# Kernel tuning notes

Measured on AMD Instinct MI355X. Metric: run time of the kernel, lower is better.

## Reference

```python
import jax, jax.numpy as jnp
import numpy as np

B, C, H, NP, M = 32, 768, 12, 196, 64
D = C // H
GRID = 14  # sqrt(196)
NG = 1 + NP  # cls + patches = 197
EPS = 1e-5


def _ln(x, w, b):
    mu = x.mean(-1, keepdims=True)
    var = ((x - mu) ** 2).mean(-1, keepdims=True)
    return (x - mu) * jax.lax.rsqrt(var + EPS) * w + b


def setup_inputs() -> dict:
    key = jax.random.key(0)
    ks = jax.random.split(key, 14)
    std = 0.02
    return {
        "x": jax.random.normal(ks[0], (B, NG + M, C), dtype=jnp.float32),
        "ps": jax.random.uniform(ks[1], (B, M, 2), dtype=jnp.float32) * 224.0,
        "ns": jax.random.randint(ks[2], (B,), 1, M + 1, dtype=jnp.int32),
        "norm1_w": jnp.ones((C,), jnp.float32),
        "norm1_b": jnp.zeros((C,), jnp.float32),
        "qkv_w": jax.random.normal(ks[3], (3 * C, C), jnp.float32) * std,
        "proj_w": jax.random.normal(ks[4], (C, C), jnp.float32) * std,
        "proj_b": jnp.zeros((C,), jnp.float32),
        "norm2_w": jnp.ones((C,), jnp.float32),
        "norm2_b": jnp.zeros((C,), jnp.float32),
        "fc1_w": jax.random.normal(ks[5], (4 * C, C), jnp.float32) * std,
        "fc1_b": jnp.zeros((4 * C,), jnp.float32),
        "fc2_w": jax.random.normal(ks[6], (C, 4 * C), jnp.float32) * std,
        "fc2_b": jnp.zeros((C,), jnp.float32),
    }


def reference(x, ps, ns, norm1_w, norm1_b, qkv_w, proj_w, proj_b,
              norm2_w, norm2_b, fc1_w, fc1_b, fc2_w, fc2_b):
    Bn, Nt, Cd = x.shape  # Nt = 1 + 196 + M
    scale = D ** -0.5

    h = _ln(x, norm1_w, norm1_b)
    qkv = (h @ qkv_w.T).reshape(Bn, Nt, 3, H, D).transpose(2, 0, 3, 1, 4)  # [3,B,H,Nt,D]
    q, k, v = qkv[0], qkv[1], qkv[2]

    # ---- global attention over cls + patch tokens (first 197) ----
    attn = jnp.einsum('bhnd,bhmd->bhnm', q[:, :, :NG], k[:, :, :NG]) * scale
    attn = jax.nn.softmax(attn, axis=-1)
    xg = jnp.einsum('bhnm,bhmd->bhnd', attn, v[:, :, :NG])
    xg = xg.transpose(0, 2, 1, 3).reshape(Bn, NG, Cd)  # [B,197,C]

    # ---- keypoint bilinear-gather attention (get_single_filter_matrix) ----
    pos = ps / 16.0  # [B,M,2]; pos[...,1] -> row (dim 4), pos[...,0] -> col (dim 5)
    c0 = jnp.clip(jnp.floor(pos[..., 0]), 0, GRID - 1).astype(jnp.int32)
    c1 = jnp.clip(jnp.ceil(pos[..., 0]), 0, GRID - 1).astype(jnp.int32)
    r0 = jnp.clip(jnp.floor(pos[..., 1]), 0, GRID - 1).astype(jnp.int32)
    r1 = jnp.clip(jnp.ceil(pos[..., 1]), 0, GRID - 1).astype(jnp.int32)
    # neighbor order: top_left, top_right, bottom_left, bottom_right
    rows = jnp.stack([r0, r1, r0, r1], axis=-1)  # [B,M,4]
    cols = jnp.stack([c0, c0, c1, c1], axis=-1)
    flat = rows * GRID + cols  # [B,M,4] flat index into 196 patch tokens

    kp = k[:, :, 1:NG]  # [B,H,196,D]
    vp = v[:, :, 1:NG]
    idx = jnp.broadcast_to(flat.reshape(Bn, 1, M * 4, 1), (Bn, H, M * 4, D))
    knb = jnp.take_along_axis(kp, idx, axis=2).reshape(Bn, H, M, 4, D)
    vnb = jnp.take_along_axis(vp, idx, axis=2).reshape(Bn, H, M, 4, D)

    qk = q[:, :, NG:]  # keypoint queries [B,H,M,D]
    a = jnp.einsum('bhmd,bhmjd->bhmj', qk, knb)  # no scale, per original
    a = jax.nn.softmax(a, axis=-1)
    kout = jnp.einsum('bhmj,bhmjd->bhmd', a, vnb)
    kout = kout.transpose(0, 2, 1, 3).reshape(Bn, M, Cd)

    y = jnp.concatenate([xg, kout], axis=1) @ proj_w.T + proj_b
    x = x + y

    h2 = _ln(x, norm2_w, norm2_b)
    h2 = jax.nn.gelu(h2 @ fc1_w.T + fc1_b, approximate=False)
    x = x + (h2 @ fc2_w.T + fc2_b)
    return x
```

## Files before the change

kernel.cpp:

```cpp
#include <hip/hip_runtime.h>

typedef unsigned short u16;
typedef unsigned int u32;
typedef u16 u16x8 __attribute__((ext_vector_type(8)));
typedef u16 u16x4 __attribute__((ext_vector_type(4)));
typedef float f32x4 __attribute__((ext_vector_type(4)));
typedef __bf16 bf16x8 __attribute__((ext_vector_type(8)));

#define NHEAD 12
#define NT 261
#define NGL 197
#define CDIM 768
#define KT 14
#define PS_STRIDE 232
#define VT_STRIDE 232

__device__ __forceinline__ float bf2f(u16 u) {
    u32 x = ((u32)u) << 16;
    float f;
    __builtin_memcpy(&f, &x, 4);
    return f;
}
__device__ __forceinline__ u16 f2bf(float f) {
    u32 x;
    __builtin_memcpy(&x, &f, 4);
    x = (x + 0x7fffu + ((x >> 16) & 1u)) >> 16;
    return (u16)x;
}

#define GLD_LDS16(g, l) \
    __builtin_amdgcn_global_load_lds((const __attribute__((address_space(1))) void*)(g), \
                                     (__attribute__((address_space(3))) void*)(l), 16, 0, 0)
#define WAITV(n) asm volatile("s_waitcnt vmcnt(" #n ")" ::: "memory")
#define BARM() asm volatile("s_barrier" ::: "memory")

struct CvArgs {
    const float* in[4];
    u16* out[4];
    int n4[4];
};

__device__ __forceinline__ void ln_row(const float* __restrict__ in, const float* __restrict__ w,
                                       const float* __restrict__ bia, u16* __restrict__ out,
                                       int row, int lane) {
    const float4* r = (const float4*)(in + (size_t)row * CDIM);
    float4 a = r[lane], b4 = r[lane + 64], c4 = r[lane + 128];
    float s  = a.x + a.y + a.z + a.w + b4.x + b4.y + b4.z + b4.w + c4.x + c4.y + c4.z + c4.w;
    float ss = a.x*a.x + a.y*a.y + a.z*a.z + a.w*a.w
             + b4.x*b4.x + b4.y*b4.y + b4.z*b4.z + b4.w*b4.w
             + c4.x*c4.x + c4.y*c4.y + c4.z*c4.z + c4.w*c4.w;
#pragma unroll
    for (int off = 32; off; off >>= 1) {
        s  += __shfl_xor(s, off);
        ss += __shfl_xor(ss, off);
    }
    float mu = s * (1.f / 768.f);
    float var = ss * (1.f / 768.f) - mu * mu;
    float inv = rsqrtf(var + 1e-5f);
    const float4* wp = (const float4*)w;
    const float4* bp = (const float4*)bia;
    u16* o = out + (size_t)row * CDIM;
#pragma unroll
    for (int t = 0; t < 3; ++t) {
        float4 v = (t == 0) ? a : (t == 1) ? b4 : c4;
        float4 ww = wp[lane + t * 64], bb = bp[lane + t * 64];
        u16x4 ov;
        ov[0] = f2bf((v.x - mu) * inv * ww.x + bb.x);
        ov[1] = f2bf((v.y - mu) * inv * ww.y + bb.y);
        ov[2] = f2bf((v.z - mu) * inv * ww.z + bb.z);
        ov[3] = f2bf((v.w - mu) * inv * ww.w + bb.w);
        *(u16x4*)(o + t * 256 + lane * 4) = ov;
    }
}

__global__ __launch_bounds__(256) void pre_k(const float* __restrict__ x, const float* __restrict__ w,
                                             const float* __restrict__ bia, u16* __restrict__ out,
                                             int nrows, CvArgs cv) {
    if (blockIdx.y == 0) {
        int i = blockIdx.x * 256 + threadIdx.x;
        int s0 = cv.n4[0], s1 = s0 + cv.n4[1], s2 = s1 + cv.n4[2], s3 = s2 + cv.n4[3];
        const float* in;
        u16* o;
        int base;
        if (i < s0)      { in = cv.in[0]; o = cv.out[0]; base = 0; }
        else if (i < s1) { in = cv.in[1]; o = cv.out[1]; base = s0; }
        else if (i < s2) { in = cv.in[2]; o = cv.out[2]; base = s1; }
        else if (i < s3) { in = cv.in[3]; o = cv.out[3]; base = s2; }
        else return;
        int j = i - base;
        float4 v = ((const float4*)in)[j];
        u16x4 ov;
        ov[0] = f2bf(v.x); ov[1] = f2bf(v.y); ov[2] = f2bf(v.z); ov[3] = f2bf(v.w);
        ((u16x4*)o)[j] = ov;
    } else {
        int lane = threadIdx.x & 63, wv = threadIdx.x >> 6;
        int row = blockIdx.x * 4 + wv;
        if (row < nrows) ln_row(x, w, bia, out, row, lane);
    }
}

__global__ __launch_bounds__(256) void ln_w(const float* __restrict__ in, const float* __restrict__ w,
                                            const float* __restrict__ bia, u16* __restrict__ out, int nrows) {
    int lane = threadIdx.x & 63, wv = threadIdx.x >> 6;
    int row = blockIdx.x * 4 + wv;
    if (row < nrows) ln_row(in, w, bia, out, row, lane);
}

template <int EPI>
__global__ __launch_bounds__(256, 4) void gemm11(const u16* __restrict__ A, const u16* __restrict__ Bw,
                                                 int M, int N, int K, int nbn,
                                                 const float* __restrict__ bias,
                                                 const float* __restrict__ resid, void* __restrict__ outp) {
    __shared__ __align__(16) u16 sm[2][8192];
    const int tid = threadIdx.x;
    const int nwg = gridDim.x;
    const int q = nwg >> 3, r = nwg & 7;
    const int xcd = blockIdx.x & 7, within = blockIdx.x >> 3;
    const int id2 = (xcd < r ? xcd * (q + 1) : r * (q + 1) + (xcd - r) * q) + within;
    const int bm = id2 / nbn, bn = id2 % nbn;
    const int lane = tid & 63, wv = tid >> 6;
    const int wr = wv >> 1, wc = wv & 1;
    const int l15 = lane & 15, lg = lane >> 4;
    const int arow0 = bm * 128, brow0 = bn * 128;
    const int nt = K >> 5;

    const int srow = tid >> 2;
    const int sslot = tid & 3;
    const int sk = (sslot ^ ((srow >> 1) & 3)) * 8;
    const u16* gA[2];
    const u16* gB[2];
#pragma unroll
    for (int i = 0; i < 2; ++i) {
        int ar = arow0 + i * 64 + srow;
        if (ar >= M) ar = M - 1;
        gA[i] = A + (size_t)ar * K + sk;
        gB[i] = Bw + (size_t)(brow0 + i * 64 + srow) * K + sk;
    }

    auto STAGE = [&](int tt) {
        u16* sb = sm[tt & 1];
        const size_t ko = (size_t)tt * 32;
#pragma unroll
        for (int i = 0; i < 2; ++i) GLD_LDS16(gA[i] + ko, sb + i * 2048 + tid * 8);
#pragma unroll
        for (int i = 0; i < 2; ++i) GLD_LDS16(gB[i] + ko, sb + 4096 + i * 2048 + tid * 8);
    };

    f32x4 acc[4][4] = {};
    const int xb = (l15 >> 1) & 3;

    STAGE(0);
    for (int t = 0; t < nt; ++t) {
        if (t + 1 < nt) {
            STAGE(t + 1);
            WAITV(4);
        } else {
            WAITV(0);
        }
        BARM();
        const u16* sb = sm[t & 1];
        bf16x8 af[4], bq[4];
#pragma unroll
        for (int mi = 0; mi < 4; ++mi)
            af[mi] = *(const bf16x8*)(sb + (wr * 64 + mi * 16 + l15) * 32 + ((lg ^ xb) * 8));
#pragma unroll
        for (int ni = 0; ni < 4; ++ni)
            bq[ni] = *(const bf16x8*)(sb + 4096 + (wc * 64 + ni * 16 + l15) * 32 + ((lg ^ xb) * 8));
#pragma unroll
        for (int mi = 0; mi < 4; ++mi)
#pragma unroll
            for (int ni = 0; ni < 4; ++ni)
                acc[mi][ni] = __builtin_amdgcn_mfma_f32_16x16x32_bf16(af[mi], bq[ni], acc[mi][ni], 0, 0, 0);
        if (t + 2 < nt) BARM();
    }

#pragma unroll
    for (int mi = 0; mi < 4; ++mi) {
        int row0 = arow0 + wr * 64 + mi * 16 + lg * 4;
#pragma unroll
        for (int ni = 0; ni < 4; ++ni) {
            int col = brow0 + wc * 64 + ni * 16 + l15;
            float bb = (EPI == 0) ? 0.f : bias[col];
#pragma unroll
            for (int rr = 0; rr < 4; ++rr) {
                int row = row0 + rr;
                if (row < M) {
                    float v = acc[mi][ni][rr] + bb;
                    if (EPI == 2) {
                        float z = v + 0.044715f * v * v * v;
                        v = v / (1.f + __expf(-1.5957691216f * z));
                    }
                    ((u16*)outp)[(size_t)row * N + col] = f2bf(v);
                }
            }
        }
    }
}

__global__ __launch_bounds__(256, 4) void gemm12(const u16* __restrict__ A, const u16* __restrict__ Bw,
                                                 int M, int N, int K, int nbn,
                                                 const float* __restrict__ bias,
                                                 const float* __restrict__ resid, void* __restrict__ outp) {
    __shared__ __align__(16) u16 sm[2][6144];
    const int tid = threadIdx.x;
    const int nwg = gridDim.x;
    const int q = nwg >> 3, r = nwg & 7;
    const int xcd = blockIdx.x & 7, within = blockIdx.x >> 3;
    const int id2 = (xcd < r ? xcd * (q + 1) : r * (q + 1) + (xcd - r) * q) + within;
    const int bm = id2 / nbn, bn = id2 % nbn;
    const int lane = tid & 63, wv = tid >> 6;
    const int wr = wv >> 1, wc = wv & 1;
    const int l15 = lane & 15, lg = lane >> 4;
    const int arow0 = bm * 64, brow0 = bn * 128;
    const int nt = K >> 5;

    const int srow = tid >> 2;
    const int sslot = tid & 3;
    const int sk = (sslot ^ ((srow >> 1) & 3)) * 8;
    int ar0 = arow0 + srow; if (ar0 >= M) ar0 = M - 1;
    const u16* gA0 = A + (size_t)ar0 * K + sk;
    const u16* gB[2];
#pragma unroll
    for (int i = 0; i < 2; ++i)
        gB[i] = Bw + (size_t)(brow0 + i * 64 + srow) * K + sk;

    auto STAGE = [&](int tt) {
        u16* sb = sm[tt & 1];
        const size_t ko = (size_t)tt * 32;
        GLD_LDS16(gA0 + ko, sb + tid * 8);
#pragma unroll
        for (int i = 0; i < 2; ++i) GLD_LDS16(gB[i] + ko, sb + 2048 + i * 2048 + tid * 8);
    };

    f32x4 acc[2][4] = {};
    const int xb = (l15 >> 1) & 3;

    STAGE(0);
    for (int t = 0; t < nt; ++t) {
        if (t + 1 < nt) {
            STAGE(t + 1);
            WAITV(3);
        } else {
            WAITV(0);
        }
        BARM();
        const u16* sb = sm[t & 1];
        bf16x8 af[2], bq[4];
#pragma unroll
        for (int mi = 0; mi < 2; ++mi)
            af[mi] = *(const bf16x8*)(sb + (wr * 32 + mi * 16 + l15) * 32 + ((lg ^ xb) * 8));
#pragma unroll
        for (int ni = 0; ni < 4; ++ni)
            bq[ni] = *(const bf16x8*)(sb + 2048 + (wc * 64 + ni * 16 + l15) * 32 + ((lg ^ xb) * 8));
#pragma unroll
        for (int mi = 0; mi < 2; ++mi)
#pragma unroll
            for (int ni = 0; ni < 4; ++ni)
                acc[mi][ni] = __builtin_amdgcn_mfma_f32_16x16x32_bf16(af[mi], bq[ni], acc[mi][ni], 0, 0, 0);
        if (t + 2 < nt) BARM();
    }

#pragma unroll
    for (int mi = 0; mi < 2; ++mi) {
        int row0 = arow0 + wr * 32 + mi * 16 + lg * 4;
#pragma unroll
        for (int ni = 0; ni < 4; ++ni) {
            int col = brow0 + wc * 64 + ni * 16 + l15;
            float bb = bias[col];
#pragma unroll
            for (int rr = 0; rr < 4; ++rr) {
                int row = row0 + rr;
                if (row < M) {
                    float v = acc[mi][ni][rr] + bb + resid[(size_t)row * N + col];
                    ((float*)outp)[(size_t)row * N + col] = v;
                }
            }
        }
    }
}

__global__ __launch_bounds__(256) void attn_fused(const u16* __restrict__ qkv, const float* __restrict__ ps,
                                                  u16* __restrict__ Z) {
    __shared__ __align__(16) u16 lds0[4 * 16 * PS_STRIDE];
    __shared__ __align__(16) u16 Vt[64 * VT_STRIDE];
    const int tid = threadIdx.x;
    const int lane = tid & 63, wv = tid >> 6;

    if (blockIdx.x >= 1536) {
        int idx = blockIdx.x - 1536;
        int b = idx >> 4;
        int m = (idx & 15) * 4 + wv;
        float px = ps[((size_t)b * 64 + m) * 2 + 0] * (1.f / 16.f);
        float py = ps[((size_t)b * 64 + m) * 2 + 1] * (1.f / 16.f);
        int c0 = min(max((int)floorf(px), 0), 13);
        int c1 = min(max((int)ceilf(px), 0), 13);
        int r0 = min(max((int)floorf(py), 0), 13);
        int r1 = min(max((int)ceilf(py), 0), 13);
        int tok[4];
        tok[0] = 1 + r0 * 14 + c0;
        tok[1] = 1 + r1 * 14 + c0;
        tok[2] = 1 + r0 * 14 + c1;
        tok[3] = 1 + r1 * 14 + c1;
        const size_t rowq = ((size_t)b * NT + NGL + m) * 2304;
#pragma unroll 1
        for (int h = 0; h < NHEAD; ++h) {
            float qv = bf2f(qkv[rowq + h * 64 + lane]);
            float a[4];
#pragma unroll
            for (int j = 0; j < 4; ++j) {
                float p = qv * bf2f(qkv[((size_t)b * NT + tok[j]) * 2304 + 768 + h * 64 + lane]);
#pragma unroll
                for (int off = 32; off; off >>= 1) p += __shfl_xor(p, off);
                a[j] = p;
            }
            float mx = fmaxf(fmaxf(a[0], a[1]), fmaxf(a[2], a[3]));
            float e0 = expf(a[0] - mx), e1 = expf(a[1] - mx), e2 = expf(a[2] - mx), e3 = expf(a[3] - mx);
            float inv = 1.f / (e0 + e1 + e2 + e3);
            float v0 = bf2f(qkv[((size_t)b * NT + tok[0]) * 2304 + 1536 + h * 64 + lane]);
            float v1 = bf2f(qkv[((size_t)b * NT + tok[1]) * 2304 + 1536 + h * 64 + lane]);
            float v2 = bf2f(qkv[((size_t)b * NT + tok[2]) * 2304 + 1536 + h * 64 + lane]);
            float v3 = bf2f(qkv[((size_t)b * NT + tok[3]) * 2304 + 1536 + h * 64 + lane]);
            float o = (e0 * v0 + e1 * v1 + e2 * v2 + e3 * v3) * inv;
            Z[((size_t)b * NT + NGL + m) * CDIM + h * 64 + lane] = f2bf(o);
        }
        return;
    }

    const int blk = blockIdx.x;
    const int qt = blk & 3;
    const int bh = blk >> 2;
    const int h = bh % NHEAD, b = bh / NHEAD;
    const int l15 = lane & 15, lg = lane >> 4;
    const u16* base = qkv + (size_t)b * NT * 2304;

    for (int c = tid; c < 224 * 8; c += 256) {
        int row = c >> 3, ch = c & 7;
        u16x8 v = {};
        if (row < NGL) v = *(const u16x8*)(base + (size_t)row * 2304 + 768 + h * 64 + ch * 8);
        int byte = row * 128 + ((ch * 16) ^ ((row & 7) << 4));
        *(u16x8*)((char*)lds0 + byte) = v;
    }
    for (int c = tid; c < 112 * 8; c += 256) {
        int mp = c >> 3, dch = c & 7;
        int m0 = mp * 2;
        u16x8 a0 = {}, a1 = {};
        if (m0 < NGL)     a0 = *(const u16x8*)(base + (size_t)m0 * 2304 + 1536 + h * 64 + dch * 8);
        if (m0 + 1 < NGL) a1 = *(const u16x8*)(base + (size_t)(m0 + 1) * 2304 + 1536 + h * 64 + dch * 8);
#pragma unroll
        for (int j = 0; j < 8; ++j) {
            u32 pk = (u32)a0[j] | ((u32)a1[j] << 16);
            *(u32*)((char*)Vt + (size_t)(dch * 8 + j) * (VT_STRIDE * 2) + m0 * 2) = pk;
        }
    }
    const int q0 = qt * 64 + wv * 16;
    int qrow = q0 + l15; if (qrow > NGL - 1) qrow = NGL - 1;
    bf16x8 aq0 = *(const bf16x8*)(base + (size_t)qrow * 2304 + h * 64 + lg * 8);
    bf16x8 aq1 = *(const bf16x8*)(base + (size_t)qrow * 2304 + h * 64 + 32 + lg * 8);
    __syncthreads();

    f32x4 s[KT];
    const int sw = (l15 & 7) << 4;
#pragma unroll
    for (int t = 0; t < KT; ++t) {
        const char* krow = (const char*)lds0 + (t * 16 + l15) * 128;
        bf16x8 bk0 = *(const bf16x8*)(krow + ((lg * 16) ^ sw));
        bf16x8 bk1 = *(const bf16x8*)(krow + ((64 + lg * 16) ^ sw));
        f32x4 acc = {};
        acc = __builtin_amdgcn_mfma_f32_16x16x32_bf16(aq0, bk0, acc, 0, 0, 0);
        acc = __builtin_amdgcn_mfma_f32_16x16x32_bf16(aq1, bk1, acc, 0, 0, 0);
        s[t] = acc * 0.125f;
    }
    float mx[4] = {-1e30f, -1e30f, -1e30f, -1e30f};
#pragma unroll
    for (int t = 0; t < KT; ++t)
#pragma unroll
        for (int r = 0; r < 4; ++r) mx[r] = fmaxf(mx[r], s[t][r]);
#pragma unroll
    for (int off = 1; off < 16; off <<= 1)
#pragma unroll
        for (int r = 0; r < 4; ++r) mx[r] = fmaxf(mx[r], __shfl_xor(mx[r], off));
    float sum[4] = {};
#pragma unroll
    for (int t = 0; t < KT; ++t) {
        bool valid = (t * 16 + l15) < NGL;
#pragma unroll
        for (int r = 0; r < 4; ++r) {
            float e = valid ? __expf(s[t][r] - mx[r]) : 0.f;
            s[t][r] = e;
            sum[r] += e;
        }
    }
#pragma unroll
    for (int off = 1; off < 16; off <<= 1)
#pragma unroll
        for (int r = 0; r < 4; ++r) sum[r] += __shfl_xor(sum[r], off);
    float inv[4];
#pragma unroll
    for (int r = 0; r < 4; ++r) inv[r] = 1.f / sum[r];

    __syncthreads();
    u16* Pw = lds0 + wv * 16 * PS_STRIDE;
#pragma unroll
    for (int t = 0; t < KT; ++t)
#pragma unroll
        for (int r = 0; r < 4; ++r)
            Pw[(4 * lg + r) * PS_STRIDE + t * 16 + l15] = f2bf(s[t][r] * inv[r]);

    f32x4 o[4] = {};
#pragma unroll
    for (int ks = 0; ks < 7; ++ks) {
        bf16x8 pa = *(const bf16x8*)(Pw + l15 * PS_STRIDE + ks * 32 + lg * 8);
#pragma unroll
        for (int dt = 0; dt < 4; ++dt) {
            bf16x8 bv = *(const bf16x8*)((const char*)Vt + (size_t)(dt * 16 + l15) * (VT_STRIDE * 2) + ks * 64 + lg * 16);
            o[dt] = __builtin_amdgcn_mfma_f32_16x16x32_bf16(pa, bv, o[dt], 0, 0, 0);
        }
    }
#pragma unroll
    for (int dt = 0; dt < 4; ++dt)
#pragma unroll
        for (int r = 0; r < 4; ++r) {
            int q = q0 + 4 * lg + r;
            if (q < NGL) Z[((size_t)b * NT + q) * CDIM + h * 64 + dt * 16 + l15] = f2bf(o[dt][r]);
        }
}

extern "C" void kernel_launch(void* const* d_in, const int* in_sizes, int n_in,
                              void* d_out, int out_size, void* d_ws, size_t ws_size,
                              hipStream_t stream) {
    const float* x      = (const float*)d_in[0];
    const float* ps     = (const float*)d_in[1];
    const float* n1w    = (const float*)d_in[3];
    const float* n1b    = (const float*)d_in[4];
    const float* qkv_w  = (const float*)d_in[5];
    const float* proj_w = (const float*)d_in[6];
    const float* proj_b = (const float*)d_in[7];
    const float* n2w    = (const float*)d_in[8];
    const float* n2b    = (const float*)d_in[9];
    const float* fc1_w  = (const float*)d_in[10];
    const float* fc1_b  = (const float*)d_in[11];
    const float* fc2_w  = (const float*)d_in[12];
    const float* fc2_b  = (const float*)d_in[13];

    char* ws = (char*)d_ws;
    const int M = 32 * NT;
    u16* hbuf  = (u16*)ws;
    u16* qkvb  = (u16*)(ws + 12828672);
    u16* Zb    = (u16*)(ws + 12828672 + 38486016);
    u16* Gb    = (u16*)(ws + 12828672);
    float* x1  = (float*)(ws + 64143360);
    u16* wq    = (u16*)(ws + 89800704);
    u16* wp    = wq + 2304 * 768;
    u16* w1    = wp + 768 * 768;
    u16* w2    = w1 + 3072 * 768;

    CvArgs cv;
    cv.in[0] = qkv_w;  cv.out[0] = wq; cv.n4[0] = 2304 * 768 / 4;
    cv.in[1] = proj_w; cv.out[1] = wp; cv.n4[1] = 768 * 768 / 4;
    cv.in[2] = fc1_w;  cv.out[2] = w1; cv.n4[2] = 3072 * 768 / 4;
    cv.in[3] = fc2_w;  cv.out[3] = w2; cv.n4[3] = 768 * 3072 / 4;

    pre_k<<<dim3(6912, 2), 256, 0, stream>>>(x, n1w, n1b, hbuf, M, cv);
    gemm11<0><<<66 * 18, 256, 0, stream>>>(hbuf, wq, M, 2304, 768, 18, nullptr, nullptr, qkvb);
    attn_fused<<<2048, 256, 0, stream>>>(qkvb, ps, Zb);
    gemm12<<<131 * 6, 256, 0, stream>>>(Zb, wp, M, 768, 768, 6, proj_b, x, x1);
    ln_w<<<2088, 256, 0, stream>>>(x1, n2w, n2b, hbuf, M);
    gemm11<2><<<66 * 24, 256, 0, stream>>>(hbuf, w1, M, 3072, 768, 24, fc1_b, nullptr, Gb);
    gemm12<<<131 * 6, 256, 0, stream>>>(Gb, w2, M, 768, 3072, 6, fc2_b, x1, (float*)d_out);
}
```

Before: 304.2 us.

## Skip unused K/V rows in QKV GEMM, store residual x1 as bf16

The QKV projection becomes a dedicated kernel. Q is computed for all 261 tokens, but K and V only for the 197 global tokens, using a row remap (row/197*261 + row%197), because keypoint tokens never serve as keys or values. The proj and fc2 GEMMs move from 64-row tiles to the 128-row gemm11 tiles, and the intermediate residual x1 is stored in bf16 rather than fp32, with a bf16-input LayerNorm to match. This cuts MMA work and memory traffic, but rounding the residual stream to bf16 costs precision, and the larger tiles give fewer blocks for the N=768 GEMMs.

```diff
diff --git a/kernel.cpp b/kernel.cpp
--- a/kernel.cpp
+++ b/kernel.cpp
@@ -69,6 +69,43 @@
         ov[1] = f2bf((v.y - mu) * inv * ww.y + bb.y);
         ov[2] = f2bf((v.z - mu) * inv * ww.z + bb.z);
         ov[3] = f2bf((v.w - mu) * inv * ww.w + bb.w);
+        *(u16x4*)(o + t * 256 + lane * 4) = ov;
+    }
+}
+
+__device__ __forceinline__ void ln_row_bf(const u16* __restrict__ in, const float* __restrict__ w,
+                                          const float* __restrict__ bia, u16* __restrict__ out,
+                                          int row, int lane) {
+    const u16* r = in + (size_t)row * CDIM;
+    float v[12];
+#pragma unroll
+    for (int t = 0; t < 3; ++t) {
+        u16x4 u = *(const u16x4*)(r + t * 256 + lane * 4);
+#pragma unroll
+        for (int j = 0; j < 4; ++j) v[t * 4 + j] = bf2f(u[j]);
+    }
+    float s = 0.f, ss = 0.f;
+#pragma unroll
+    for (int j = 0; j < 12; ++j) { s += v[j]; ss += v[j] * v[j]; }
+#pragma unroll
+    for (int off = 32; off; off >>= 1) {
+        s  += __shfl_xor(s, off);
+        ss += __shfl_xor(ss, off);
+    }
+    float mu = s * (1.f / 768.f);
+    float var = ss * (1.f / 768.f) - mu * mu;
+    float inv = rsqrtf(var + 1e-5f);
+    const float4* wp = (const float4*)w;
+    const float4* bp = (const float4*)bia;
+    u16* o = out + (size_t)row * CDIM;
+#pragma unroll
+    for (int t = 0; t < 3; ++t) {
+        float4 ww = wp[lane + t * 64], bb = bp[lane + t * 64];
+        u16x4 ov;
+        ov[0] = f2bf((v[t * 4 + 0] - mu) * inv * ww.x + bb.x);
+        ov[1] = f2bf((v[t * 4 + 1] - mu) * inv * ww.y + bb.y);
+        ov[2] = f2bf((v[t * 4 + 2] - mu) * inv * ww.z + bb.z);
+        ov[3] = f2bf((v[t * 4 + 3] - mu) * inv * ww.w + bb.w);
         *(u16x4*)(o + t * 256 + lane * 4) = ov;
     }
 }
@@ -99,18 +136,18 @@
     }
 }
 
-__global__ __launch_bounds__(256) void ln_w(const float* __restrict__ in, const float* __restrict__ w,
-                                            const float* __restrict__ bia, u16* __restrict__ out, int nrows) {
+__global__ __launch_bounds__(256) void ln_wbf(const u16* __restrict__ in, const float* __restrict__ w,
+                                              const float* __restrict__ bia, u16* __restrict__ out, int nrows) {
     int lane = threadIdx.x & 63, wv = threadIdx.x >> 6;
     int row = blockIdx.x * 4 + wv;
-    if (row < nrows) ln_row(in, w, bia, out, row, lane);
+    if (row < nrows) ln_row_bf(in, w, bia, out, row, lane);
 }
 
 template <int EPI>
 __global__ __launch_bounds__(256, 4) void gemm11(const u16* __restrict__ A, const u16* __restrict__ Bw,
                                                  int M, int N, int K, int nbn,
                                                  const float* __restrict__ bias,
-                                                 const float* __restrict__ resid, void* __restrict__ outp) {
+                                                 const void* __restrict__ resid, void* __restrict__ outp) {
     __shared__ __align__(16) u16 sm[2][8192];
     const int tid = threadIdx.x;
     const int nwg = gridDim.x;
@@ -180,80 +217,95 @@
 #pragma unroll
         for (int ni = 0; ni < 4; ++ni) {
             int col = brow0 + wc * 64 + ni * 16 + l15;
-            float bb = (EPI == 0) ? 0.f : bias[col];
+            float bb = bias[col];
 #pragma unroll
             for (int rr = 0; rr < 4; ++rr) {
                 int row = row0 + rr;
                 if (row < M) {
                     float v = acc[mi][ni][rr] + bb;
-                    if (EPI == 2) {
+                    if (EPI == 1) {
+                        v += ((const float*)resid)[(size_t)row * N + col];
+                        ((u16*)outp)[(size_t)row * N + col] = f2bf(v);
+                    } else if (EPI == 2) {
                         float z = v + 0.044715f * v * v * v;
                         v = v / (1.f + __expf(-1.5957691216f * z));
+                        ((u16*)outp)[(size_t)row * N + col] = f2bf(v);
+                    } else {
+                        v += bf2f(((const u16*)resid)[(size_t)row * N + col]);
+                        ((float*)outp)[(size_t)row * N + col] = v;
                     }
-                    ((u16*)outp)[(size_t)row * N + col] = f2bf(v);
                 }
             }
         }
     }
 }
 
-__global__ __launch_bounds__(256, 4) void gemm12(const u16* __restrict__ A, const u16* __restrict__ Bw,
-                                                 int M, int N, int K, int nbn,
-                                                 const float* __restrict__ bias,
-                                                 const float* __restrict__ resid, void* __restrict__ outp) {
-    __shared__ __align__(16) u16 sm[2][6144];
+__global__ __launch_bounds__(256, 4) void gemm_qkv(const u16* __restrict__ A, const u16* __restrict__ Bw,
+                                                   u16* __restrict__ outp) {
+    __shared__ __align__(16) u16 sm[2][8192];
     const int tid = threadIdx.x;
     const int nwg = gridDim.x;
     const int q = nwg >> 3, r = nwg & 7;
     const int xcd = blockIdx.x & 7, within = blockIdx.x >> 3;
     const int id2 = (xcd < r ? xcd * (q + 1) : r * (q + 1) + (xcd - r) * q) + within;
-    const int bm = id2 / nbn, bn = id2 % nbn;
+    const bool kvz = (id2 >= 396);
+    const int idz = kvz ? id2 - 396 : id2;
+    const int bm = kvz ? idz / 12 : idz / 6;
+    const int bn = kvz ? idz % 12 : idz % 6;
+    const int Mz = kvz ? 6304 : 8352;
+    const int colbase = kvz ? 768 + bn * 128 : bn * 128;
     const int lane = tid & 63, wv = tid >> 6;
     const int wr = wv >> 1, wc = wv & 1;
     const int l15 = lane & 15, lg = lane >> 4;
-    const int arow0 = bm * 64, brow0 = bn * 128;
-    const int nt = K >> 5;
+    const int arow0 = bm * 128;
+    const int K = 768;
+    const int nt = 24;
 
     const int srow = tid >> 2;
     const int sslot = tid & 3;
     const int sk = (sslot ^ ((srow >> 1) & 3)) * 8;
-    int ar0 = arow0 + srow; if (ar0 >= M) ar0 = M - 1;
-    const u16* gA0 = A + (size_t)ar0 * K + sk;
+    const u16* gA[2];
     const u16* gB[2];
 #pragma unroll
-    for (int i = 0; i < 2; ++i)
-        gB[i] = Bw + (size_t)(brow0 + i * 64 + srow) * K + sk;
+    for (int i = 0; i < 2; ++i) {
+        int ar = arow0 + i * 64 + srow;
+        if (ar >= Mz) ar = Mz - 1;
+        int real = kvz ? (ar / 197) * 261 + (ar % 197) : ar;
+        gA[i] = A + (size_t)real * K + sk;
+        gB[i] = Bw + (size_t)(colbase + i * 64 + srow) * K + sk;
+    }
 
     auto STAGE = [&](int tt) {
         u16* sb = sm[tt & 1];
         const size_t ko = (size_t)tt * 32;
-        GLD_LDS16(gA0 + ko, sb + tid * 8);
-#pragma unroll
-        for (int i = 0; i < 2; ++i) GLD_LDS16(gB[i] + ko, sb + 2048 + i * 2048 + tid * 8);
+#pragma unroll
+        for (int i = 0; i < 2; ++i) GLD_LDS16(gA[i] + ko, sb + i * 2048 + tid * 8);
+#pragma unroll
+        for (int i = 0; i < 2; ++i) GLD_LDS16(gB[i] + ko, sb + 4096 + i * 2048 + tid * 8);
     };
 
-    f32x4 acc[2][4] = {};
+    f32x4 acc[4][4] = {};
     const int xb = (l15 >> 1) & 3;
 
     STAGE(0);
     for (int t = 0; t < nt; ++t) {
         if (t + 1 < nt) {
             STAGE(t + 1);
-            WAITV(3);
+            WAITV(4);
         } else {
             WAITV(0);
         }
         BARM();
         const u16* sb = sm[t & 1];
-        bf16x8 af[2], bq[4];
-#pragma unroll
-        for (int mi = 0; mi < 2; ++mi)
-            af[mi] = *(const bf16x8*)(sb + (wr * 32 + mi * 16 + l15) * 32 + ((lg ^ xb) * 8));
+        bf16x8 af[4], bq[4];
+#pragma unroll
+        for (int mi = 0; mi < 4; ++mi)
+            af[mi] = *(const bf16x8*)(sb + (wr * 64 + mi * 16 + l15) * 32 + ((lg ^ xb) * 8));
 #pragma unroll
         for (int ni = 0; ni < 4; ++ni)
-            bq[ni] = *(const bf16x8*)(sb + 2048 + (wc * 64 + ni * 16 + l15) * 32 + ((lg ^ xb) * 8));
-#pragma unroll
-        for (int mi = 0; mi < 2; ++mi)
+            bq[ni] = *(const bf16x8*)(sb + 4096 + (wc * 64 + ni * 16 + l15) * 32 + ((lg ^ xb) * 8));
+#pragma unroll
+        for (int mi = 0; mi < 4; ++mi)
 #pragma unroll
             for (int ni = 0; ni < 4; ++ni)
                 acc[mi][ni] = __builtin_amdgcn_mfma_f32_16x16x32_bf16(af[mi], bq[ni], acc[mi][ni], 0, 0, 0);
@@ -261,18 +313,17 @@
     }
 
 #pragma unroll
-    for (int mi = 0; mi < 2; ++mi) {
-        int row0 = arow0 + wr * 32 + mi * 16 + lg * 4;
+    for (int mi = 0; mi < 4; ++mi) {
+        int row0 = arow0 + wr * 64 + mi * 16 + lg * 4;
 #pragma unroll
         for (int ni = 0; ni < 4; ++ni) {
-            int col = brow0 + wc * 64 + ni * 16 + l15;
-            float bb = bias[col];
+            int col = colbase + wc * 64 + ni * 16 + l15;
 #pragma unroll
             for (int rr = 0; rr < 4; ++rr) {
                 int row = row0 + rr;
-                if (row < M) {
-                    float v = acc[mi][ni][rr] + bb + resid[(size_t)row * N + col];
-                    ((float*)outp)[(size_t)row * N + col] = v;
+                if (row < Mz) {
+                    int real = kvz ? (row / 197) * 261 + (row % 197) : row;
+                    outp[(size_t)real * 2304 + col] = f2bf(acc[mi][ni][rr]);
                 }
             }
         }
@@ -448,7 +499,7 @@
     u16* qkvb  = (u16*)(ws + 12828672);
     u16* Zb    = (u16*)(ws + 12828672 + 38486016);
     u16* Gb    = (u16*)(ws + 12828672);
-    float* x1  = (float*)(ws + 64143360);
+    u16* x1    = (u16*)(ws + 64143360);
     u16* wq    = (u16*)(ws + 89800704);
     u16* wp    = wq + 2304 * 768;
     u16* w1    = wp + 768 * 768;
@@ -461,10 +512,10 @@
     cv.in[3] = fc2_w;  cv.out[3] = w2; cv.n4[3] = 768 * 3072 / 4;
 
     pre_k<<<dim3(6912, 2), 256, 0, stream>>>(x, n1w, n1b, hbuf, M, cv);
-    gemm11<0><<<66 * 18, 256, 0, stream>>>(hbuf, wq, M, 2304, 768, 18, nullptr, nullptr, qkvb);
+    gemm_qkv<<<996, 256, 0, stream>>>(hbuf, wq, qkvb);
     attn_fused<<<2048, 256, 0, stream>>>(qkvb, ps, Zb);
-    gemm12<<<131 * 6, 256, 0, stream>>>(Zb, wp, M, 768, 768, 6, proj_b, x, x1);
-    ln_w<<<2088, 256, 0, stream>>>(x1, n2w, n2b, hbuf, M);
+    gemm11<1><<<66 * 6, 256, 0, stream>>>(Zb, wp, M, 768, 768, 6, proj_b, x, x1);
+    ln_wbf<<<2088, 256, 0, stream>>>(x1, n2w, n2b, hbuf, M);
     gemm11<2><<<66 * 24, 256, 0, stream>>>(hbuf, w1, M, 3072, 768, 24, fc1_b, nullptr, Gb);
-    gemm12<<<131 * 6, 256, 0, stream>>>(Gb, w2, M, 768, 3072, 6, fc2_b, x1, (float*)d_out);
-}
+    gemm11<3><<<66 * 6, 256, 0, stream>>>(Gb, w2, M, 768, 3072, 6, fc2_b, x1, (float*)d_out);
+}
```

Result: faster. 269.3 us (-11.5%).
